# Optimization experiments

Measured on AMD Instinct MI355X. Metric: run time of the kernel, lower is better.

## Reference

```python
import jax, jax.numpy as jnp
import numpy as np
import math

B, S, D, H, L, F = 32, 512, 512, 8, 4, 2048
DK = D // H
EPS = 1e-5


def _cosine_pos_emb(seq_len, d_model):
    pe = np.zeros((seq_len, d_model), dtype=np.float32)
    position = np.arange(seq_len, dtype=np.float32)[:, None]
    div_term = np.exp(np.arange(0, d_model, 2, dtype=np.float32) * (-math.log(10000.0) / d_model))
    pe[:, 0::2] = np.sin(position * div_term)
    pe[:, 1::2] = np.cos(position * div_term)
    return jnp.asarray(pe[None])  # (1, S, D)


def setup_inputs() -> dict:
    key = jax.random.key(0)
    ks = jax.random.split(key, 12)
    w = 0.02
    return {
        "q_embed_data": jax.random.normal(ks[0], (B, S, D), jnp.float32),
        "qa_embed_data": jax.random.normal(ks[1], (B, S, D), jnp.float32),
        "forget_rate": jax.random.uniform(ks[2], (B, S, 1), jnp.float32),
        "pos_emb": _cosine_pos_emb(S, D),
        # per-layer stacked params (torch Linear convention: W is (out,in))
        "Wk": w * jax.random.normal(ks[3], (L, D, D), jnp.float32),
        "bk": jnp.zeros((L, D), jnp.float32),
        "Wv": w * jax.random.normal(ks[4], (L, D, D), jnp.float32),
        "bv": jnp.zeros((L, D), jnp.float32),
        "Wo": w * jax.random.normal(ks[5], (L, D, D), jnp.float32),
        "bo": jnp.zeros((L, D), jnp.float32),
        "W1": w * jax.random.normal(ks[6], (L, F, D), jnp.float32),
        "b1": jnp.zeros((L, F), jnp.float32),
        "W2": w * jax.random.normal(ks[7], (L, D, F), jnp.float32),
        "b2": jnp.zeros((L, D), jnp.float32),
        "ln1_g": jnp.ones((L, D), jnp.float32),
        "ln1_b": jnp.zeros((L, D), jnp.float32),
        "ln2_g": jnp.ones((L, D), jnp.float32),
        "ln2_b": jnp.zeros((L, D), jnp.float32),
    }


def _layer_norm(x, g, b):
    mu = jnp.mean(x, axis=-1, keepdims=True)
    var = jnp.mean(jnp.square(x - mu), axis=-1, keepdims=True)
    return (x - mu) * jax.lax.rsqrt(var + EPS) * g + b


def _forward(q_embed_data, qa_embed_data, forget_rate, pos_emb,
             Wk, bk, Wv, bv, Wo, bo, W1, b1, W2, b2,
             ln1_g, ln1_b, ln2_g, ln2_b):
    x = q_embed_data + pos_emb   # queries/keys stream
    y = qa_embed_data + pos_emb  # values stream (fixed across layers)
    scale = 1.0 / math.sqrt(DK)
    # mask=0 path: triu(k=0)==0 -> strictly past positions only (j < i)
    allowed = jnp.tril(jnp.ones((S, S), dtype=bool), k=-1)
    fr = forget_rate[:, None, :, :]  # (B,1,S,1): row-wise decay on scores
    neg = jnp.asarray(-1e32, x.dtype)

    def block(x, p):
        wk, bk_, wv, bv_, wo, bo_, w1, b1_, w2, b2_, g1, be1, g2, be2 = p
        # kq_same=1: q and k share the k_linear projection (so q == k here)
        kq = (jnp.einsum('bsd,ed->bse', x, wk) + bk_).reshape(B, S, H, DK).transpose(0, 2, 1, 3)
        v = (jnp.einsum('bsd,ed->bse', y, wv) + bv_).reshape(B, S, H, DK).transpose(0, 2, 1, 3)
        scores = jnp.einsum('bhsd,bhtd->bhst', kq, kq) * scale
        scores = scores * fr
        scores = jnp.where(allowed, scores, neg)
        attn = jax.nn.softmax(scores, axis=-1)
        attn = attn.at[:, :, 0, :].set(0.0)  # zero_pad: first query row zeroed
        ctx = jnp.einsum('bhst,bhtd->bhsd', attn, v).transpose(0, 2, 1, 3).reshape(B, S, D)
        out = jnp.einsum('bsd,ed->bse', ctx, wo) + bo_
        x = _layer_norm(x + out, g1, be1)
        ff = jnp.einsum('bsf,df->bsd', jax.nn.relu(jnp.einsum('bsd,fd->bsf', x, w1) + b1_), w2) + b2_
        x = _layer_norm(x + ff, g2, be2)
        return x, None

    x, _ = jax.lax.scan(block, x, (Wk, bk, Wv, bv, Wo, bo, W1, b1, W2, b2, ln1_g, ln1_b, ln2_g, ln2_b))
    return x


def reference(q_embed_data, qa_embed_data, forget_rate, pos_emb,
              Wk, bk, Wv, bv, Wo, bo, W1, b1, W2, b2,
              ln1_g, ln1_b, ln2_g, ln2_b):
    return _forward(q_embed_data, qa_embed_data, forget_rate, pos_emb,
                    Wk, bk, Wv, bv, Wo, bo, W1, b1, W2, b2,
                    ln1_g, ln1_b, ln2_g, ln2_b)
```

## Files before the change

### kernel.cpp

```cpp
#include <hip/hip_runtime.h>
#include <hip/hip_bf16.h>

constexpr int B_ = 32, S_ = 512, D_ = 512, H_ = 8, L_ = 4, F_ = 2048, DK_ = 64;

typedef __attribute__((ext_vector_type(8))) short short8;
typedef __attribute__((ext_vector_type(4))) float f32x4;
typedef __attribute__((ext_vector_type(16))) float f32x16;

__device__ inline unsigned short f2b(float f) {
  union { __hip_bfloat16 h; unsigned short u; } cv;
  cv.h = __float2bfloat16(f);
  return cv.u;
}
__device__ inline float b2f(unsigned short u) {
  union { unsigned int i; float f; } c;
  c.i = ((unsigned int)u) << 16;
  return c.f;
}
__device__ inline unsigned pkbf(float a, float b) {
  unsigned r;
  asm("v_cvt_pk_bf16_f32 %0, %1, %2" : "=v"(r) : "v"(a), "v"(b));
  return r;
}
__device__ inline float waveReduceSum(float v) {
  #pragma unroll
  for (int o = 32; o > 0; o >>= 1) v += __shfl_xor(v, o);
  return v;
}

__global__ void prep_kernel(const float4* __restrict__ q, const float4* __restrict__ qa,
                            const float4* __restrict__ pos,
                            uint2* __restrict__ xb, uint2* __restrict__ yb) {
  int i = blockIdx.x * blockDim.x + threadIdx.x;
  float4 p = pos[i & 65535];
  float4 a = q[i], c = qa[i];
  uint2 px, py;
  px.x = pkbf(a.x + p.x, a.y + p.y);
  px.y = pkbf(a.z + p.z, a.w + p.w);
  py.x = pkbf(c.x + p.x, c.y + p.y);
  py.y = pkbf(c.z + p.z, c.w + p.w);
  xb[i] = px;
  yb[i] = py;
}

__global__ void cast_kernel(const float4* __restrict__ src, uint2* __restrict__ dst, int n4) {
  int i = blockIdx.x * blockDim.x + threadIdx.x;
  if (i >= n4) return;
  float4 v = src[i];
  uint2 p;
  p.x = pkbf(v.x, v.y);
  p.y = pkbf(v.z, v.w);
  dst[i] = p;
}

template<int RELU, int STORE>
__global__ __launch_bounds__(256, 2) void gemm128_kernel(
    const __hip_bfloat16* __restrict__ A,
    const __hip_bfloat16* __restrict__ W,
    const float* __restrict__ bias,
    const __hip_bfloat16* __restrict__ A2,
    const __hip_bfloat16* __restrict__ W2,
    const float* __restrict__ bias2,
    __hip_bfloat16* __restrict__ Cb,
    __hip_bfloat16* __restrict__ Cb2,
    int Ndim, int Kdim, int kLen)
{
  __shared__ char lds[32768];
  const int tid = threadIdx.x, wave = tid >> 6, lane = tid & 63;
  const int rl = lane & 15, gq = lane >> 4;
  const int wr = wave >> 1, wc = wave & 1;

  const int nwg = gridDim.x * gridDim.y;
  const int lin = blockIdx.y * gridDim.x + blockIdx.x;
  const int swz = (lin & 7) * (nwg >> 3) + (lin >> 3);
  const int bx = swz % gridDim.x, by = swz / gridDim.x;

  const int row0 = by * 128;
  const int col0 = bx * 128;

  const __hip_bfloat16* Ap = A;
  const __hip_bfloat16* Wp = W;
  const float* bp = bias;
  int kOff = blockIdx.z * kLen;
  if (STORE == 3) {
    kOff = 0;
    if (blockIdx.z) { Ap = A2; Wp = W2; bp = bias2; }
  }

  f32x4 acc[4][4] = {};
  const int ntiles = kLen >> 5;

  auto stage = [&](int kt, int d) {
    const int kbase = kOff + (kt << 5);
    #pragma unroll
    for (int r = 0; r < 2; ++r) {
      int p = r * 4096 + tid * 16;
      int R = p >> 6, c = (p >> 4) & 3;
      int gc = c ^ ((R >> 1) & 3);
      const __hip_bfloat16* srcA = Ap + (size_t)(row0 + R) * Kdim + kbase + gc * 8;
      __builtin_amdgcn_global_load_lds(
          (const __attribute__((address_space(1))) void*)srcA,
          (__attribute__((address_space(3))) void*)(lds + d * 8192 + p), 16, 0, 0);
      const __hip_bfloat16* srcW = Wp + (size_t)(col0 + R) * Kdim + kbase + gc * 8;
      __builtin_amdgcn_global_load_lds(
          (const __attribute__((address_space(1))) void*)srcW,
          (__attribute__((address_space(3))) void*)(lds + 16384 + d * 8192 + p), 16, 0, 0);
    }
  };

  stage(0, 0);
  __syncthreads();
  for (int kt = 0; kt < ntiles; ++kt) {
    const int d = kt & 1;
    if (kt + 1 < ntiles) stage(kt + 1, d ^ 1);

    short8 aF[4], bF[4];
    #pragma unroll
    for (int m = 0; m < 4; ++m) {
      int rr = wr * 64 + m * 16 + rl;
      aF[m] = *(const short8*)(lds + d * 8192 + rr * 64 + ((gq ^ ((rr >> 1) & 3)) << 4));
    }
    #pragma unroll
    for (int n = 0; n < 4; ++n) {
      int rr = wc * 64 + n * 16 + rl;
      bF[n] = *(const short8*)(lds + 16384 + d * 8192 + rr * 64 + ((gq ^ ((rr >> 1) & 3)) << 4));
    }
    __builtin_amdgcn_s_setprio(1);
    #pragma unroll
    for (int m = 0; m < 4; ++m)
      #pragma unroll
      for (int n = 0; n < 4; ++n)
        acc[m][n] = __builtin_amdgcn_mfma_f32_16x16x32_bf16(aF[m], bF[n], acc[m][n], 0, 0, 0);
    __builtin_amdgcn_s_setprio(0);
    __syncthreads();
  }

  char* sw = lds + wave * 8192;
  const bool vt = (STORE == 3) && (blockIdx.z == 1);
  const bool addb = (STORE == 3) ? true : ((bias != nullptr) && (blockIdx.z == 0));
  float bvv[4];
  #pragma unroll
  for (int n = 0; n < 4; ++n)
    bvv[n] = addb ? bp[col0 + wc * 64 + n * 16 + rl] : 0.0f;

  #pragma unroll
  for (int n = 0; n < 4; ++n)
    #pragma unroll
    for (int m = 0; m < 4; ++m)
      #pragma unroll
      for (int j = 0; j < 4; ++j) {
        float val = acc[m][n][j] + bvv[n];
        if (RELU) val = fmaxf(val, 0.0f);
        int addr;
        if (vt) {
          int orow = n * 16 + rl, ocol = m * 16 + gq * 4 + j;
          addr = orow * 128 + ((ocol * 2) ^ ((orow & 7) << 4));
        } else {
          int orow = m * 16 + gq * 4 + j;
          addr = orow * 128 + (((n * 16 + rl) * 2) ^ (((orow >> 1) & 7) << 4));
        }
        *(unsigned short*)(sw + addr) = f2b(val);
      }
  asm volatile("s_waitcnt lgkmcnt(0)" ::: "memory");
  __builtin_amdgcn_sched_barrier(0);

  __hip_bfloat16* Cbd = blockIdx.z ? Cb2 : Cb;
  const int cchunk = lane & 7;
  if (vt) {
    const int bh64 = ((row0 >> 9) * 8 + (col0 >> 6) + wc) * 64;
    const int tbase = (row0 & 511) + wr * 64;
    #pragma unroll
    for (int it = 0; it < 8; ++it) {
      int d0 = it * 8 + (lane >> 3);
      uint4 vv = *(const uint4*)(sw + d0 * 128 + ((cchunk * 16) ^ ((d0 & 7) << 4)));
      *(uint4*)((char*)Cbd + ((size_t)(bh64 + d0) * 512 + tbase) * 2 + cchunk * 16) = vv;
    }
  } else {
    #pragma unroll
    for (int it = 0; it < 8; ++it) {
      int orow = it * 8 + (lane >> 3);
      uint4 vv = *(const uint4*)(sw + orow * 128 + ((cchunk * 16) ^ (((orow >> 1) & 7) << 4)));
      *(uint4*)((char*)Cbd + ((size_t)(row0 + wr * 64 + orow) * Ndim + col0 + wc * 64) * 2 +
                cchunk * 16) = vv;
    }
  }
}

__global__ __launch_bounds__(512, 2) void fattn_kernel(
    const __hip_bfloat16* __restrict__ kq,
    const __hip_bfloat16* __restrict__ vT,
    const float* __restrict__ fr,
    __hip_bfloat16* __restrict__ ctx)
{
  __shared__ char lds[131072];
  const int tid = threadIdx.x, wave = tid >> 6, lane = tid & 63;
  const int lq = lane & 31, hi = lane >> 5;
  const int bh = blockIdx.x;
  const int b = bh >> 3, h = bh & 7;
  const size_t kqbase = ((size_t)b * S_) * D_ + h * DK_;
  const size_t vtbase = ((size_t)bh * DK_) * S_;
  const char* kg = (const char*)kq + kqbase * 2;
  const char* vg = (const char*)vT + vtbase * 2;

  #pragma unroll
  for (int i = 0; i < 8; ++i) {
    int p = i * 8192 + tid * 16;
    int r = p >> 7, ck = (p >> 4) & 7;
    __builtin_amdgcn_global_load_lds(
        (const __attribute__((address_space(1))) void*)(kg + (size_t)r * 1024 + ((ck ^ (r & 7)) << 4)),
        (__attribute__((address_space(3))) void*)(lds + p), 16, 0, 0);
  }
  #pragma unroll
  for (int i = 0; i < 8; ++i) {
    int p = i * 8192 + tid * 16;
    int d = p >> 10, ck = (p >> 4) & 63;
    __builtin_amdgcn_global_load_lds(
        (const __attribute__((address_space(1))) void*)(vg + (size_t)d * 1024 + ((ck ^ (d & 15)) << 4)),
        (__attribute__((address_space(3))) void*)(lds + 65536 + p), 16, 0, 0);
  }

  const int qia = wave, qib = 15 - wave;
  const int na = qia + 1, nb = qib + 1;
  const int sa = qia * 32 + lq, sb = qib * 32 + lq;
  const float sfa = fr[b * S_ + sa] * 0.125f;
  const float sfb = fr[b * S_ + sb] * 0.125f;

  asm volatile("s_waitcnt vmcnt(0)" ::: "memory");
  __builtin_amdgcn_sched_barrier(0);
  __builtin_amdgcn_s_barrier();

  short8 qa_[4], qb_[4];
  #pragma unroll
  for (int f = 0; f < 4; ++f) {
    qa_[f] = *(const short8*)(lds + sa * 128 + ((((f << 1) + hi) ^ (sa & 7)) << 4));
    qb_[f] = *(const short8*)(lds + sb * 128 + ((((f << 1) + hi) ^ (sb & 7)) << 4));
  }

  f32x16 oa0 = {}, oa1 = {}, ob0 = {}, ob1 = {};
  float ma = -3.0e38f, la = 0.0f, mb = -3.0e38f, lb = 0.0f;

  auto process = [&](f32x16& o0, f32x16& o1, float& m, float& l,
                     const short8* qf, int srow, float sf,
                     const short8* kb, const short8* vb0, const short8* vb1,
                     int t0) {
    f32x16 s = {};
    #pragma unroll
    for (int f = 0; f < 4; ++f)
      s = __builtin_amdgcn_mfma_f32_32x32x16_bf16(kb[f], qf[f], s, 0, 0, 0);
    float p[16];
    #pragma unroll
    for (int r = 0; r < 16; ++r) {
      int tg = t0 + (r & 3) + 8 * (r >> 2) + 4 * hi;
      float v = s[r] * sf;
      p[r] = (tg >= srow) ? -3.0e38f : v;
    }
    float t8[8], t4[4];
    #pragma unroll
    for (int i = 0; i < 8; ++i) t8[i] = fmaxf(p[2 * i], p[2 * i + 1]);
    #pragma unroll
    for (int i = 0; i < 4; ++i) t4[i] = fmaxf(t8[2 * i], t8[2 * i + 1]);
    float mt = fmaxf(fmaxf(t4[0], t4[1]), fmaxf(t4[2], t4[3]));
    mt = fmaxf(mt, __shfl_xor(mt, 32));
    float mn = fmaxf(m, mt);
    float fac = __expf(m - mn);
    m = mn;
    l *= fac;
    #pragma unroll
    for (int r = 0; r < 16; ++r) p[r] = __expf(p[r] - mn);
    float s8[8], s4[4];
    #pragma unroll
    for (int i = 0; i < 8; ++i) s8[i] = p[2 * i] + p[2 * i + 1];
    #pragma unroll
    for (int i = 0; i < 4; ++i) s4[i] = s8[2 * i] + s8[2 * i + 1];
    float ps = (s4[0] + s4[1]) + (s4[2] + s4[3]);
    ps += __shfl_xor(ps, 32);
    l += ps;
    #pragma unroll
    for (int i = 0; i < 16; ++i) { o0[i] *= fac; o1[i] *= fac; }
    #pragma unroll
    for (int c = 0; c < 2; ++c) {
      unsigned X0 = pkbf(p[8 * c + 0], p[8 * c + 1]);
      unsigned X1 = pkbf(p[8 * c + 2], p[8 * c + 3]);
      unsigned Y0 = pkbf(p[8 * c + 4], p[8 * c + 5]);
      unsigned Y1 = pkbf(p[8 * c + 6], p[8 * c + 7]);
      unsigned z0 = hi ? X0 : Y0, z1 = hi ? X1 : Y1;
      unsigned r0 = __shfl_xor(z0, 32), r1 = __shfl_xor(z1, 32);
      union { unsigned u[4]; short8 v; } pb;
      pb.u[0] = hi ? r0 : X0;
      pb.u[1] = hi ? r1 : X1;
      pb.u[2] = hi ? Y0 : r0;
      pb.u[3] = hi ? Y1 : r1;
      o0 = __builtin_amdgcn_mfma_f32_32x32x16_bf16(vb0[c], pb.v, o0, 0, 0, 0);
      o1 = __builtin_amdgcn_mfma_f32_32x32x16_bf16(vb1[c], pb.v, o1, 0, 0, 0);
    }
  };

  for (int ti = 0; ti < nb; ++ti) {
    const int t0 = ti * 32;
    short8 kb[4];
    #pragma unroll
    for (int f = 0; f < 4; ++f) {
      int tw = t0 + lq;
      kb[f] = *(const short8*)(lds + tw * 128 + ((((f << 1) + hi) ^ (tw & 7)) << 4));
    }
    short8 vb0[2], vb1[2];
    #pragma unroll
    for (int c = 0; c < 2; ++c) {
      int ck = 4 * ti + 2 * c + hi;
      int d0 = lq;
      vb0[c] = *(const short8*)(lds + 65536 + d0 * 1024 + ((ck ^ (d0 & 15)) << 4));
      int d1 = 32 + lq;
      vb1[c] = *(const short8*)(lds + 65536 + d1 * 1024 + ((ck ^ (d1 & 15)) << 4));
    }
    if (ti < na) process(oa0, oa1, ma, la, qa_, sa, sfa, kb, vb0, vb1, t0);
    process(ob0, ob1, mb, lb, qb_, sb, sfb, kb, vb0, vb1, t0);
  }

  auto writeO = [&](const f32x16& o0, const f32x16& o1, float l, int srow) {
    float inv = (srow == 0) ? 0.0f : 1.0f / l;
    char* base = (char*)ctx + (((size_t)(b * S_ + srow)) * D_ + h * DK_) * 2;
    #pragma unroll
    for (int gg = 0; gg < 4; ++gg) {
      uint2 w0, w1;
      w0.x = pkbf(o0[4 * gg + 0] * inv, o0[4 * gg + 1] * inv);
      w0.y = pkbf(o0[4 * gg + 2] * inv, o0[4 * gg + 3] * inv);
      *(uint2*)(base + (8 * gg + 4 * hi) * 2) = w0;
      w1.x = pkbf(o1[4 * gg + 0] * inv, o1[4 * gg + 1] * inv);
      w1.y = pkbf(o1[4 * gg + 2] * inv, o1[4 * gg + 3] * inv);
      *(uint2*)(base + (32 + 8 * gg + 4 * hi) * 2) = w1;
    }
  };
  writeO(oa0, oa1, la, sa);
  writeO(ob0, ob1, lb, sb);
}

template<int NADD, int FINAL>
__global__ __launch_bounds__(256) void ln_kernel(
    const uint4* __restrict__ xres, const uint4* __restrict__ add,
    const uint4* __restrict__ add2,
    const float* __restrict__ g, const float* __restrict__ bta,
    uint4* __restrict__ xb_out, float4* __restrict__ xf_out)
{
  const int lane = threadIdx.x & 63, wv = threadIdx.x >> 6;
  const size_t row = (size_t)blockIdx.x * 4 + wv;

  uint4 xr = xres[row * 64 + lane];
  uint4 ab = add[row * 64 + lane];
  const unsigned short* xp = (const unsigned short*)&xr;
  const unsigned short* ap = (const unsigned short*)&ab;
  float v[8];
  #pragma unroll
  for (int i = 0; i < 8; ++i) v[i] = b2f(xp[i]) + b2f(ap[i]);
  if (NADD == 2) {
    uint4 ab2 = add2[row * 64 + lane];
    const unsigned short* ap2 = (const unsigned short*)&ab2;
    #pragma unroll
    for (int i = 0; i < 8; ++i) v[i] += b2f(ap2[i]);
  }
  float s = 0.0f;
  #pragma unroll
  for (int i = 0; i < 8; ++i) s += v[i];
  s = waveReduceSum(s);
  float mu = s * (1.0f / 512.0f);
  float vs = 0.0f;
  #pragma unroll
  for (int i = 0; i < 8; ++i) { float dd = v[i] - mu; vs += dd * dd; }
  vs = waveReduceSum(vs);
  float rstd = rsqrtf(vs * (1.0f / 512.0f) + 1e-5f);

  const int c0i = lane * 8;
  float4 gg0 = *(const float4*)(g + c0i), gg1 = *(const float4*)(g + c0i + 4);
  float4 bb0 = *(const float4*)(bta + c0i), bb1 = *(const float4*)(bta + c0i + 4);
  float o[8];
  o[0] = (v[0] - mu) * rstd * gg0.x + bb0.x;
  o[1] = (v[1] - mu) * rstd * gg0.y + bb0.y;
  o[2] = (v[2] - mu) * rstd * gg0.z + bb0.z;
  o[3] = (v[3] - mu) * rstd * gg0.w + bb0.w;
  o[4] = (v[4] - mu) * rstd * gg1.x + bb1.x;
  o[5] = (v[5] - mu) * rstd * gg1.y + bb1.y;
  o[6] = (v[6] - mu) * rstd * gg1.z + bb1.z;
  o[7] = (v[7] - mu) * rstd * gg1.w + bb1.w;

  if (FINAL) {
    float4 w0, w1;
    w0.x = o[0]; w0.y = o[1]; w0.z = o[2]; w0.w = o[3];
    w1.x = o[4]; w1.y = o[5]; w1.z = o[6]; w1.w = o[7];
    xf_out[row * 128 + lane * 2] = w0;
    xf_out[row * 128 + lane * 2 + 1] = w1;
  } else {
    uint4 pw;
    pw.x = pkbf(o[0], o[1]);
    pw.y = pkbf(o[2], o[3]);
    pw.z = pkbf(o[4], o[5]);
    pw.w = pkbf(o[6], o[7]);
    xb_out[row * 64 + lane] = pw;
  }
}

extern "C" void kernel_launch(void* const* d_in, const int* in_sizes, int n_in,
                              void* d_out, int out_size, void* d_ws, size_t ws_size,
                              hipStream_t stream) {
  (void)in_sizes; (void)n_in; (void)out_size; (void)ws_size;
  const float* q   = (const float*)d_in[0];
  const float* qa  = (const float*)d_in[1];
  const float* frr = (const float*)d_in[2];
  const float* pos = (const float*)d_in[3];
  const float* Wk  = (const float*)d_in[4];
  const float* bk  = (const float*)d_in[5];
  const float* Wv  = (const float*)d_in[6];
  const float* bv  = (const float*)d_in[7];
  const float* Wo  = (const float*)d_in[8];
  const float* bo  = (const float*)d_in[9];
  const float* W1  = (const float*)d_in[10];
  const float* b1  = (const float*)d_in[11];
  const float* W2  = (const float*)d_in[12];
  const float* b2  = (const float*)d_in[13];
  const float* g1  = (const float*)d_in[14];
  const float* be1 = (const float*)d_in[15];
  const float* g2  = (const float*)d_in[16];
  const float* be2 = (const float*)d_in[17];

  char* ws = (char*)d_ws;
  __hip_bfloat16* xb   = (__hip_bfloat16*)(ws + 33554432);
  __hip_bfloat16* yb   = (__hip_bfloat16*)(ws + 50331648);
  __hip_bfloat16* kqb  = (__hip_bfloat16*)(ws + 67108864);
  __hip_bfloat16* vtb  = (__hip_bfloat16*)(ws + 83886080);
  __hip_bfloat16* ctxb = (__hip_bfloat16*)(ws + 100663296);
  __hip_bfloat16* hb   = (__hip_bfloat16*)(ws + 117440512);
  __hip_bfloat16* wkb  = (__hip_bfloat16*)(ws + 184549376);
  __hip_bfloat16* wvb  = (__hip_bfloat16*)(ws + 186646528);
  __hip_bfloat16* wob  = (__hip_bfloat16*)(ws + 188743680);
  __hip_bfloat16* w1b  = (__hip_bfloat16*)(ws + 190840832);
  __hip_bfloat16* w2b  = (__hip_bfloat16*)(ws + 199229440);
  __hip_bfloat16* obf = (__hip_bfloat16*)(ws + 67108864);
  __hip_bfloat16* pf0 = (__hip_bfloat16*)(ws + 83886080);
  __hip_bfloat16* pf1 = (__hip_bfloat16*)(ws + 100663296);

  prep_kernel<<<8192, 256, 0, stream>>>((const float4*)q, (const float4*)qa,
                                        (const float4*)pos, (uint2*)xb, (uint2*)yb);
  cast_kernel<<<1024, 256, 0, stream>>>((const float4*)Wk, (uint2*)wkb, 262144);
  cast_kernel<<<1024, 256, 0, stream>>>((const float4*)Wv, (uint2*)wvb, 262144);
  cast_kernel<<<1024, 256, 0, stream>>>((const float4*)Wo, (uint2*)wob, 262144);
  cast_kernel<<<4096, 256, 0, stream>>>((const float4*)W1, (uint2*)w1b, 1048576);
  cast_kernel<<<4096, 256, 0, stream>>>((const float4*)W2, (uint2*)w2b, 1048576);

  for (int l = 0; l < L_; ++l) {
    gemm128_kernel<0,3><<<dim3(4, 128, 2), 256, 0, stream>>>(
        xb, wkb + (size_t)l * 262144, bk + l * 512,
        yb, wvb + (size_t)l * 262144, bv + l * 512,
        kqb, vtb, 512, 512, 512);
    fattn_kernel<<<256, 512, 0, stream>>>(kqb, vtb, frr, ctxb);
    gemm128_kernel<0,0><<<dim3(4, 128, 1), 256, 0, stream>>>(
        ctxb, wob + (size_t)l * 262144, bo + l * 512,
        nullptr, nullptr, nullptr, obf, nullptr, 512, 512, 512);
    ln_kernel<1,0><<<4096, 256, 0, stream>>>(
        (const uint4*)xb, (const uint4*)obf, nullptr,
        g1 + l * 512, be1 + l * 512, (uint4*)xb, nullptr);
    gemm128_kernel<1,0><<<dim3(16, 128, 1), 256, 0, stream>>>(
        xb, w1b + (size_t)l * 1048576, b1 + l * 2048,
        nullptr, nullptr, nullptr, hb, nullptr, 2048, 512, 512);
    gemm128_kernel<0,0><<<dim3(4, 128, 2), 256, 0, stream>>>(
        hb, w2b + (size_t)l * 1048576, b2 + l * 512,
        nullptr, nullptr, nullptr, pf0, pf1, 512, 2048, 1024);
    if (l == L_ - 1) {
      ln_kernel<2,1><<<4096, 256, 0, stream>>>(
          (const uint4*)xb, (const uint4*)pf0, (const uint4*)pf1,
          g2 + l * 512, be2 + l * 512, nullptr, (float4*)d_out);
    } else {
      ln_kernel<2,0><<<4096, 256, 0, stream>>>(
          (const uint4*)xb, (const uint4*)pf0, (const uint4*)pf1,
          g2 + l * 512, be2 + l * 512, (uint4*)xb, nullptr);
    }
  }
}
```

Before: 734.5 us.

## Deepen GEMM LDS pipeline to four stages and drop FFN2 split-K

The GEMM kernel's LDS staging grows from a double buffer to a 4-deep ring (64KB). It prefetches three tiles ahead, using explicit vmcnt waits and a single barrier per iteration in place of two syncthreads. This is meant to hide global-load latency better. The FFN2 GEMM no longer splits K across two partial outputs, so the second LayerNorm reads one partial sum, which cuts partial-output traffic but halves that GEMM's grid. Doubling LDS to 64KB may lower occupancy below the launch-bounds target of 2 blocks.

```diff
diff --git a/kernel.cpp b/kernel.cpp
--- a/kernel.cpp
+++ b/kernel.cpp
@@ -65,7 +65,7 @@
     __hip_bfloat16* __restrict__ Cb2,
     int Ndim, int Kdim, int kLen)
 {
-  __shared__ char lds[32768];
+  __shared__ char lds[65536];
   const int tid = threadIdx.x, wave = tid >> 6, lane = tid & 63;
   const int rl = lane & 15, gq = lane >> 4;
   const int wr = wave >> 1, wc = wave & 1;
@@ -90,7 +90,8 @@
   f32x4 acc[4][4] = {};
   const int ntiles = kLen >> 5;
 
-  auto stage = [&](int kt, int d) {
+  auto stage = [&](int kt) {
+    const int buf = kt & 3;
     const int kbase = kOff + (kt << 5);
     #pragma unroll
     for (int r = 0; r < 2; ++r) {
@@ -100,30 +101,40 @@
       const __hip_bfloat16* srcA = Ap + (size_t)(row0 + R) * Kdim + kbase + gc * 8;
       __builtin_amdgcn_global_load_lds(
           (const __attribute__((address_space(1))) void*)srcA,
-          (__attribute__((address_space(3))) void*)(lds + d * 8192 + p), 16, 0, 0);
+          (__attribute__((address_space(3))) void*)(lds + buf * 8192 + p), 16, 0, 0);
       const __hip_bfloat16* srcW = Wp + (size_t)(col0 + R) * Kdim + kbase + gc * 8;
       __builtin_amdgcn_global_load_lds(
           (const __attribute__((address_space(1))) void*)srcW,
-          (__attribute__((address_space(3))) void*)(lds + 16384 + d * 8192 + p), 16, 0, 0);
+          (__attribute__((address_space(3))) void*)(lds + 32768 + buf * 8192 + p), 16, 0, 0);
     }
   };
 
-  stage(0, 0);
-  __syncthreads();
+  stage(0); stage(1); stage(2);
   for (int kt = 0; kt < ntiles; ++kt) {
-    const int d = kt & 1;
-    if (kt + 1 < ntiles) stage(kt + 1, d ^ 1);
-
+    if (kt + 2 < ntiles) {
+      asm volatile("s_waitcnt vmcnt(8)" ::: "memory");
+    } else if (kt + 1 < ntiles) {
+      asm volatile("s_waitcnt vmcnt(4)" ::: "memory");
+    } else {
+      asm volatile("s_waitcnt vmcnt(0)" ::: "memory");
+    }
+    __builtin_amdgcn_sched_barrier(0);
+    __builtin_amdgcn_s_barrier();
+    __builtin_amdgcn_sched_barrier(0);
+    if (kt + 3 < ntiles) stage(kt + 3);
+
+    const int abase = (kt & 3) * 8192;
+    const int wbase = 32768 + (kt & 3) * 8192;
     short8 aF[4], bF[4];
     #pragma unroll
     for (int m = 0; m < 4; ++m) {
       int rr = wr * 64 + m * 16 + rl;
-      aF[m] = *(const short8*)(lds + d * 8192 + rr * 64 + ((gq ^ ((rr >> 1) & 3)) << 4));
+      aF[m] = *(const short8*)(lds + abase + rr * 64 + ((gq ^ ((rr >> 1) & 3)) << 4));
     }
     #pragma unroll
     for (int n = 0; n < 4; ++n) {
       int rr = wc * 64 + n * 16 + rl;
-      bF[n] = *(const short8*)(lds + 16384 + d * 8192 + rr * 64 + ((gq ^ ((rr >> 1) & 3)) << 4));
+      bF[n] = *(const short8*)(lds + wbase + rr * 64 + ((gq ^ ((rr >> 1) & 3)) << 4));
     }
     __builtin_amdgcn_s_setprio(1);
     #pragma unroll
@@ -132,8 +143,8 @@
       for (int n = 0; n < 4; ++n)
         acc[m][n] = __builtin_amdgcn_mfma_f32_16x16x32_bf16(aF[m], bF[n], acc[m][n], 0, 0, 0);
     __builtin_amdgcn_s_setprio(0);
-    __syncthreads();
-  }
+  }
+  __syncthreads();
 
   char* sw = lds + wave * 8192;
   const bool vt = (STORE == 3) && (blockIdx.z == 1);
@@ -434,7 +445,6 @@
   __hip_bfloat16* w2b  = (__hip_bfloat16*)(ws + 199229440);
   __hip_bfloat16* obf = (__hip_bfloat16*)(ws + 67108864);
   __hip_bfloat16* pf0 = (__hip_bfloat16*)(ws + 83886080);
-  __hip_bfloat16* pf1 = (__hip_bfloat16*)(ws + 100663296);
 
   prep_kernel<<<8192, 256, 0, stream>>>((const float4*)q, (const float4*)qa,
                                         (const float4*)pos, (uint2*)xb, (uint2*)yb);
@@ -459,16 +469,16 @@
     gemm128_kernel<1,0><<<dim3(16, 128, 1), 256, 0, stream>>>(
         xb, w1b + (size_t)l * 1048576, b1 + l * 2048,
         nullptr, nullptr, nullptr, hb, nullptr, 2048, 512, 512);
-    gemm128_kernel<0,0><<<dim3(4, 128, 2), 256, 0, stream>>>(
+    gemm128_kernel<0,0><<<dim3(4, 128, 1), 256, 0, stream>>>(
         hb, w2b + (size_t)l * 1048576, b2 + l * 512,
-        nullptr, nullptr, nullptr, pf0, pf1, 512, 2048, 1024);
+        nullptr, nullptr, nullptr, pf0, nullptr, 512, 2048, 2048);
     if (l == L_ - 1) {
-      ln_kernel<2,1><<<4096, 256, 0, stream>>>(
-          (const uint4*)xb, (const uint4*)pf0, (const uint4*)pf1,
+      ln_kernel<1,1><<<4096, 256, 0, stream>>>(
+          (const uint4*)xb, (const uint4*)pf0, nullptr,
           g2 + l * 512, be2 + l * 512, nullptr, (float4*)d_out);
     } else {
-      ln_kernel<2,0><<<4096, 256, 0, stream>>>(
-          (const uint4*)xb, (const uint4*)pf0, (const uint4*)pf1,
+      ln_kernel<1,0><<<4096, 256, 0, stream>>>(
+          (const uint4*)xb, (const uint4*)pf0, nullptr,
           g2 + l * 512, be2 + l * 512, (uint4*)xb, nullptr);
     }
   }
```

After: 755.2 us. 1.03x slower.
